# Kernel optimization log

Measured on AMD Instinct MI355X. Metric: run time of the kernel, lower is better.

The kernel has to match this reference:

```python
import jax, jax.numpy as jnp
import numpy as np

N = 50000       # nodes
E = 800000      # edges
D_IN = 128
D_OUT = 128
K = 3           # num_stacks
T = 2           # num_layers


def setup_inputs() -> dict:
    key = jax.random.key(0)
    ks = jax.random.split(key, 10)
    feats = jax.random.normal(ks[0], (N, D_IN), dtype=jnp.float32)
    src = jax.random.randint(ks[1], (E,), 0, N, dtype=jnp.int32)
    dst = jax.random.randint(ks[2], (E,), 0, N, dtype=jnp.int32)
    s = 0.05
    w0 = jax.random.normal(ks[3], (K, D_IN, D_OUT), dtype=jnp.float32) * s
    b0 = jax.random.normal(ks[4], (K, D_OUT), dtype=jnp.float32) * s
    w = jax.random.normal(ks[5], (K, D_OUT, D_OUT), dtype=jnp.float32) * s
    bw = jax.random.normal(ks[6], (K, D_OUT), dtype=jnp.float32) * s
    v = jax.random.normal(ks[7], (K, D_IN, D_OUT), dtype=jnp.float32) * s
    bv = jax.random.normal(ks[8], (K, D_OUT), dtype=jnp.float32) * s
    return {"feats": feats, "src": src, "dst": dst,
            "w0": w0, "b0": b0, "w": w, "bw": bw, "v": v, "bv": bv}


def _propagate(h, src, dst, norm):
    # symmetric degree-normalized SpMM: D^{-1/2} A D^{-1/2} h
    h = h * norm                                   # [N, d]
    agg = jax.ops.segment_sum(h[src], dst, num_segments=N)  # gather + scatter-add
    return agg * norm


def reference(feats, src, dst, w0, b0, w, bw, v, bv):
    ones = jnp.ones((E,), dtype=feats.dtype)
    deg = jnp.clip(jax.ops.segment_sum(ones, dst, num_segments=N), 1.0)
    norm = (deg ** -0.5)[:, None]                  # [N, 1]

    out = jnp.zeros((N, D_OUT), dtype=feats.dtype)
    for k in range(K):
        h = feats
        for t in range(T):
            h = _propagate(h, src, dst, norm)
            if t == 0:
                h = h @ w0[k] + b0[k]
            else:
                h = h @ w[k] + bw[k]
            h = h + (feats @ v[k] + bv[k])         # dropout is identity (p=0, eval)
            h = jax.nn.relu(h)
        out = out + h
    return out / K
```

## Files before the change

### kernel.cpp

```cpp
#include <hip/hip_runtime.h>

#define N_NODES 50000
#define N_EDGES 800000
#define D 128
#define PLANE ((size_t)N_NODES * D)
#define NCHUNK ((N_NODES + 255) / 256)

typedef float f32x4 __attribute__((ext_vector_type(4)));
typedef short bf16x8 __attribute__((ext_vector_type(8)));

__device__ __forceinline__ unsigned short f2bf(float x) {
  unsigned int u = __float_as_uint(x);
  u += 0x7FFFu + ((u >> 16) & 1u);
  return (unsigned short)(u >> 16);
}
__device__ __forceinline__ float bf2f(unsigned short h) {
  return __uint_as_float((unsigned int)h << 16);
}


__global__ __launch_bounds__(256) void scan_local(const int* __restrict__ cnt,
                                                  int* __restrict__ local,
                                                  int* __restrict__ partial) {
  __shared__ int s[256];
  int t = threadIdx.x;
  int i = blockIdx.x * 256 + t;
  int v = (i < N_NODES) ? cnt[i] : 0;
  s[t] = v;
  __syncthreads();
  for (int off = 1; off < 256; off <<= 1) {
    int tmp = (t >= off) ? s[t - off] : 0;
    __syncthreads();
    s[t] += tmp;
    __syncthreads();
  }
  if (i < N_NODES) local[i] = s[t] - v;
  if (t == 255) partial[blockIdx.x] = s[255];
}

__global__ __launch_bounds__(256) void scan_chunks(const int* __restrict__ partial,
                                                   int* __restrict__ chunk_off,
                                                   int* __restrict__ rowptr) {
  __shared__ int s[256];
  int t = threadIdx.x;
  int v = (t < NCHUNK) ? partial[t] : 0;
  s[t] = v;
  __syncthreads();
  for (int off = 1; off < 256; off <<= 1) {
    int tmp = (t >= off) ? s[t - off] : 0;
    __syncthreads();
    s[t] += tmp;
    __syncthreads();
  }
  if (t < NCHUNK) chunk_off[t] = s[t] - v;
  if (t == 255) rowptr[N_NODES] = s[255];
}

__global__ __launch_bounds__(256) void finalize_rows(const int* __restrict__ cnt,
                                                     const int* __restrict__ local,
                                                     const int* __restrict__ chunk_off,
                                                     int* __restrict__ rowptr,
                                                     int* __restrict__ cursor,
                                                     float* __restrict__ norm) {
  int i = blockIdx.x * 256 + threadIdx.x;
  if (i < N_NODES) {
    int r = local[i] + chunk_off[blockIdx.x];
    rowptr[i] = r;
    cursor[i] = r;
    int d = cnt[i];
    if (d < 1) d = 1;
    norm[i] = rsqrtf((float)d);
  }
}

__global__ __launch_bounds__(256) void fill_csr(const int* __restrict__ src,
                                                const int* __restrict__ dst,
                                                int* __restrict__ cursor,
                                                int* __restrict__ col) {
  int e = blockIdx.x * blockDim.x + threadIdx.x;
  if (e < N_EDGES) {
    int pos = atomicAdd(&cursor[dst[e]], 1);
    col[pos] = src[e];
  }
}


#define CONV_THREADS ((int)(PLANE / 4))
#define WT_THREADS (2 * 3 * 128 * 256)
#define PREP_TOTAL (CONV_THREADS + WT_THREADS + N_EDGES)

__global__ __launch_bounds__(256) void prep_all(const float* __restrict__ feats,
                                                const float* __restrict__ w0,
                                                const float* __restrict__ w,
                                                const float* __restrict__ v,
                                                const int* __restrict__ dst,
                                                unsigned short* __restrict__ feats_bf,
                                                unsigned short* __restrict__ bt_h1,
                                                unsigned short* __restrict__ bt_out,
                                                int* __restrict__ cnt) {
  int idx = blockIdx.x * 256 + threadIdx.x;
  if (idx < CONV_THREADS) {
    float4 x = ((const float4*)feats)[idx];
    ushort4 o;
    o.x = f2bf(x.x);
    o.y = f2bf(x.y);
    o.z = f2bf(x.z);
    o.w = f2bf(x.w);
    ((ushort4*)feats_bf)[idx] = o;
    return;
  }
  idx -= CONV_THREADS;
  if (idx < WT_THREADS) {
    int buf = idx / 98304;
    int rem = idx - buf * 98304;
    int stack = rem / 32768;
    int rem2 = rem & 32767;
    int n = rem2 >> 8;
    int k = rem2 & 255;
    const float* srcm;
    int kk;
    if (k < 128) {
      srcm = (buf == 0) ? w0 : w;
      kk = k;
    } else {
      srcm = v;
      kk = k - 128;
    }
    float val = srcm[(size_t)stack * 16384 + (size_t)kk * 128 + n];
    unsigned short* dstb = (buf == 0) ? bt_h1 : bt_out;
    dstb[(size_t)stack * 32768 + (size_t)n * 256 + k] = f2bf(val);
    return;
  }
  idx -= WT_THREADS;
  if (idx < N_EDGES) atomicAdd(&cnt[dst[idx]], 1);
}


template <int NK>
__global__ __launch_bounds__(256) void spmm_bf(const unsigned short* __restrict__ h,
                                               const float* __restrict__ norm,
                                               const int* __restrict__ rowptr,
                                               const int* __restrict__ col,
                                               unsigned short* __restrict__ out) {
  int row = blockIdx.x * 4 + (threadIdx.x >> 6);
  if (row >= N_NODES) return;
  int lane = threadIdx.x & 63;
  int sub = lane >> 4;
  int c16 = lane & 15;
  int beg = rowptr[row], end = rowptr[row + 1];

  float acc[NK][8];
#pragma unroll
  for (int m = 0; m < NK; ++m)
#pragma unroll
    for (int j = 0; j < 8; ++j) acc[m][j] = 0.f;

#pragma unroll 4
  for (int e = beg; e < end; e += 4) {
    int eidx = e + sub;
    bool valid = eidx < end;
    int s = valid ? col[eidx] : 0;
    float wgt = valid ? norm[s] : 0.f;
    const unsigned short* hp = h + (size_t)s * D + c16 * 8;
#pragma unroll
    for (int m = 0; m < NK; ++m) {
      bf16x8 hv = *(const bf16x8*)(hp + m * PLANE);
#pragma unroll
      for (int j = 0; j < 8; ++j)
        acc[m][j] = fmaf(wgt, bf2f((unsigned short)hv[j]), acc[m][j]);
    }
  }

#pragma unroll
  for (int m = 0; m < NK; ++m)
#pragma unroll
    for (int j = 0; j < 8; ++j) {
      float vv = acc[m][j];
      vv += __shfl_xor(vv, 16);
      vv += __shfl_xor(vv, 32);
      acc[m][j] = vv;
    }

  if (sub == 0) {
    float nd = norm[row];
#pragma unroll
    for (int m = 0; m < NK; ++m) {
      bf16x8 ov;
#pragma unroll
      for (int j = 0; j < 8; ++j) ov[j] = (short)f2bf(acc[m][j] * nd);
      *(bf16x8*)(out + m * PLANE + (size_t)row * D + c16 * 8) = ov;
    }
  }
}


__device__ __forceinline__ void stage_B128(unsigned short (*Bs)[256],
                                           const unsigned short* __restrict__ Btg,
                                           int tid) {
#pragma unroll
  for (int i = 0; i < 16; ++i) {
    int t = tid + i * 256;
    int n = t >> 5;
    int kc = t & 31;
    int kcs = kc ^ (n & 31);
    *(bf16x8*)&Bs[n][kcs * 8] = *(const bf16x8*)(Btg + (size_t)n * 256 + kc * 8);
  }
}

__device__ __forceinline__ bf16x8 read_B128(const unsigned short (*Bs)[256], int n,
                                            int chunk) {
  return *(const bf16x8*)&Bs[n][(chunk ^ (n & 31)) * 8];
}

__global__ __launch_bounds__(256) void gemm_h1_fused(
    const unsigned short* __restrict__ P,
    const unsigned short* __restrict__ feats_bf,
    const unsigned short* __restrict__ Bt,
    const float* __restrict__ b0, const float* __restrict__ bv,
    unsigned short* __restrict__ h1_bf) {
  __shared__ unsigned short Bs[128][256];

  int tid = threadIdx.x;
  int lane = tid & 63;
  int wv = tid >> 6;
  int ln15 = lane & 15;
  int g = lane >> 4;

  int m0 = blockIdx.x * 64 + wv * 16;
  int r0 = m0 + ln15;
  if (r0 >= N_NODES) r0 = N_NODES - 1;

  bf16x8 a0[8];
#pragma unroll
  for (int s = 0; s < 4; ++s) {
    a0[s] = *(const bf16x8*)(P + (size_t)r0 * 128 + g * 8 + s * 32);
    a0[s + 4] = *(const bf16x8*)(feats_bf + (size_t)r0 * 128 + g * 8 + s * 32);
  }

  for (int stk = 0; stk < 3; ++stk) {
    if (stk) __syncthreads();
    stage_B128(Bs, Bt + (size_t)stk * 32768, tid);
    __syncthreads();

    f32x4 acc[8];
#pragma unroll
    for (int nt = 0; nt < 8; ++nt) acc[nt] = (f32x4)(0.f);

#pragma unroll
    for (int s = 0; s < 8; ++s) {
#pragma unroll
      for (int nt = 0; nt < 8; ++nt) {
        bf16x8 bfr = read_B128(Bs, nt * 16 + ln15, s * 4 + g);
        acc[nt] = __builtin_amdgcn_mfma_f32_16x16x32_bf16(a0[s], bfr, acc[nt], 0, 0, 0);
      }
    }

    unsigned short* outp = h1_bf + (size_t)stk * PLANE;
#pragma unroll
    for (int nt = 0; nt < 8; ++nt) {
      int colj = nt * 16 + ln15;
      float bsum = b0[stk * 128 + colj] + bv[stk * 128 + colj];
#pragma unroll
      for (int r = 0; r < 4; ++r) {
        int mA = m0 + g * 4 + r;
        if (mA < N_NODES) {
          float x = acc[nt][r] + bsum;
          outp[(size_t)mA * 128 + colj] = f2bf(x > 0.f ? x : 0.f);
        }
      }
    }
  }
}

__global__ __launch_bounds__(256) void gemm_out_fused(
    const unsigned short* __restrict__ agg,
    const unsigned short* __restrict__ feats_bf,
    const unsigned short* __restrict__ Bt,
    const float* __restrict__ bwp, const float* __restrict__ bvp,
    float* __restrict__ outp) {
  __shared__ unsigned short Bs[128][256];

  int tid = threadIdx.x;
  int lane = tid & 63;
  int wv = tid >> 6;
  int ln15 = lane & 15;
  int g = lane >> 4;

  int m0 = blockIdx.x * 64 + wv * 16;
  int r0 = m0 + ln15;
  if (r0 >= N_NODES) r0 = N_NODES - 1;

  bf16x8 f0[4];
#pragma unroll
  for (int s = 0; s < 4; ++s)
    f0[s] = *(const bf16x8*)(feats_bf + (size_t)r0 * 128 + g * 8 + s * 32);

  f32x4 sum[8];
#pragma unroll
  for (int nt = 0; nt < 8; ++nt) sum[nt] = (f32x4)(0.f);

  for (int stk = 0; stk < 3; ++stk) {
    if (stk) __syncthreads();
    stage_B128(Bs, Bt + (size_t)stk * 32768, tid);
    __syncthreads();

    const unsigned short* A1 = agg + (size_t)stk * PLANE;
    bf16x8 g0[4];
#pragma unroll
    for (int s = 0; s < 4; ++s)
      g0[s] = *(const bf16x8*)(A1 + (size_t)r0 * 128 + g * 8 + s * 32);

    f32x4 acc[8];
#pragma unroll
    for (int nt = 0; nt < 8; ++nt) acc[nt] = (f32x4)(0.f);

#pragma unroll
    for (int s = 0; s < 8; ++s) {
      bf16x8 af = (s < 4) ? g0[s & 3] : f0[s & 3];
#pragma unroll
      for (int nt = 0; nt < 8; ++nt) {
        bf16x8 bfr = read_B128(Bs, nt * 16 + ln15, s * 4 + g);
        acc[nt] = __builtin_amdgcn_mfma_f32_16x16x32_bf16(af, bfr, acc[nt], 0, 0, 0);
      }
    }

#pragma unroll
    for (int nt = 0; nt < 8; ++nt) {
      int colj = nt * 16 + ln15;
      float bsum = bwp[stk * 128 + colj] + bvp[stk * 128 + colj];
#pragma unroll
      for (int r = 0; r < 4; ++r) {
        float x = acc[nt][r] + bsum;
        sum[nt][r] += (x > 0.f ? x : 0.f);
      }
    }
  }

  const float sc = 1.0f / 3.0f;
#pragma unroll
  for (int nt = 0; nt < 8; ++nt) {
    int colj = nt * 16 + ln15;
#pragma unroll
    for (int r = 0; r < 4; ++r) {
      int mA = m0 + g * 4 + r;
      if (mA < N_NODES) outp[(size_t)mA * 128 + colj] = sum[nt][r] * sc;
    }
  }
}


extern "C" void kernel_launch(void* const* d_in, const int* in_sizes, int n_in,
                              void* d_out, int out_size, void* d_ws, size_t ws_size,
                              hipStream_t stream) {
  const float* feats = (const float*)d_in[0];
  const int* src = (const int*)d_in[1];
  const int* dst = (const int*)d_in[2];
  const float* w0 = (const float*)d_in[3];
  const float* b0 = (const float*)d_in[4];
  const float* w = (const float*)d_in[5];
  const float* bw = (const float*)d_in[6];
  const float* v = (const float*)d_in[7];
  const float* bv = (const float*)d_in[8];
  float* out = (float*)d_out;

  char* ws = (char*)d_ws;
  size_t off = 0;
  auto alloc = [&](size_t bytes) {
    void* p = ws + off;
    off += (bytes + 255) & ~(size_t)255;
    return p;
  };
  int* cnt = (int*)alloc(N_NODES * 4);
  int* local = (int*)alloc(N_NODES * 4);
  int* partial = (int*)alloc(NCHUNK * 4);
  int* chunk_off = (int*)alloc(NCHUNK * 4);
  float* norm = (float*)alloc(N_NODES * 4);
  int* rowptr = (int*)alloc((N_NODES + 1) * 4);
  int* cursor = (int*)alloc(N_NODES * 4);
  int* col = (int*)alloc(N_EDGES * 4);
  unsigned short* bt_h1 = (unsigned short*)alloc(3 * 32768 * 2);
  unsigned short* bt_out = (unsigned short*)alloc(3 * 32768 * 2);

  size_t pb = PLANE * 2;
  unsigned short* feats_bf = (unsigned short*)alloc(pb);
  unsigned short* P_bf = (unsigned short*)alloc(pb);
  unsigned short* h1_bf = (unsigned short*)alloc(3 * pb);
  unsigned short* agg_bf = (unsigned short*)alloc(3 * pb);

  hipMemsetAsync(cnt, 0, N_NODES * 4, stream);

  dim3 blk(256);
  prep_all<<<(PREP_TOTAL + 255) / 256, blk, 0, stream>>>(feats, w0, w, v, dst, feats_bf,
                                                         bt_h1, bt_out, cnt);
  scan_local<<<NCHUNK, blk, 0, stream>>>(cnt, local, partial);
  scan_chunks<<<1, blk, 0, stream>>>(partial, chunk_off, rowptr);
  finalize_rows<<<NCHUNK, blk, 0, stream>>>(cnt, local, chunk_off, rowptr, cursor, norm);
  fill_csr<<<(N_EDGES + 255) / 256, blk, 0, stream>>>(src, dst, cursor, col);

  int sblocks = (N_NODES + 3) / 4;
  int mblocks64 = (N_NODES + 63) / 64;

  spmm_bf<1><<<sblocks, blk, 0, stream>>>(feats_bf, norm, rowptr, col, P_bf);
  gemm_h1_fused<<<mblocks64, blk, 0, stream>>>(P_bf, feats_bf, bt_h1, b0, bv, h1_bf);
  spmm_bf<3><<<sblocks, blk, 0, stream>>>(h1_bf, norm, rowptr, col, agg_bf);
  gemm_out_fused<<<mblocks64, blk, 0, stream>>>(agg_bf, feats_bf, bt_out, bw, bv, out);
}
```

Measured before the change: 358.1 us.

## Precompute feats@V once per stack and overlap it with first SpMM

The feats@V product used to be recomputed inside both fused GEMMs by concatenating K=256. It is now computed once per stack into a fragment-ordered bf16 buffer. That work runs in a hybrid kernel whose extra blocks perform the first SpMM at the same time. Both later GEMMs then drop to K=128 and read the precomputed values in the epilogue, and the buffers are aliased to reuse memory. In exchange, the FV buffer adds extra global traffic, and rounding the FV term to bf16 adds a small precision loss.

Measured after the change: 394.3 us. 10.1% more time.

```diff
diff --git a/kernel.cpp b/kernel.cpp
--- a/kernel.cpp
+++ b/kernel.cpp
@@ -5,6 +5,8 @@
 #define D 128
 #define PLANE ((size_t)N_NODES * D)
 #define NCHUNK ((N_NODES + 255) / 256)
+#define MB64 ((N_NODES + 63) / 64)
+#define FVB_ELEMS ((size_t)3 * MB64 * 256 * 32)
 
 typedef float f32x4 __attribute__((ext_vector_type(4)));
 typedef short bf16x8 __attribute__((ext_vector_type(8)));
@@ -86,7 +88,7 @@
 
 
 #define CONV_THREADS ((int)(PLANE / 4))
-#define WT_THREADS (2 * 3 * 128 * 256)
+#define WT_THREADS (3 * 3 * 128 * 128)
 #define PREP_TOTAL (CONV_THREADS + WT_THREADS + N_EDGES)
 
 __global__ __launch_bounds__(256) void prep_all(const float* __restrict__ feats,
@@ -95,8 +97,9 @@
                                                 const float* __restrict__ v,
                                                 const int* __restrict__ dst,
                                                 unsigned short* __restrict__ feats_bf,
-                                                unsigned short* __restrict__ bt_h1,
-                                                unsigned short* __restrict__ bt_out,
+                                                unsigned short* __restrict__ btw0,
+                                                unsigned short* __restrict__ btw,
+                                                unsigned short* __restrict__ btv,
                                                 int* __restrict__ cnt) {
   int idx = blockIdx.x * 256 + threadIdx.x;
   if (idx < CONV_THREADS) {
@@ -111,24 +114,16 @@
   }
   idx -= CONV_THREADS;
   if (idx < WT_THREADS) {
-    int buf = idx / 98304;
-    int rem = idx - buf * 98304;
-    int stack = rem / 32768;
-    int rem2 = rem & 32767;
-    int n = rem2 >> 8;
-    int k = rem2 & 255;
-    const float* srcm;
-    int kk;
-    if (k < 128) {
-      srcm = (buf == 0) ? w0 : w;
-      kk = k;
-    } else {
-      srcm = v;
-      kk = k - 128;
-    }
-    float val = srcm[(size_t)stack * 16384 + (size_t)kk * 128 + n];
-    unsigned short* dstb = (buf == 0) ? bt_h1 : bt_out;
-    dstb[(size_t)stack * 32768 + (size_t)n * 256 + k] = f2bf(val);
+    int buf = idx / 49152;
+    int rem = idx - buf * 49152;
+    int stack = rem >> 14;
+    int r2 = rem & 16383;
+    int n = r2 >> 7;
+    int k = r2 & 127;
+    const float* srcm = (buf == 0) ? w0 : (buf == 1) ? w : v;
+    unsigned short* dstb = (buf == 0) ? btw0 : (buf == 1) ? btw : btv;
+    dstb[(size_t)stack * 16384 + (size_t)n * 128 + k] =
+        f2bf(srcm[(size_t)stack * 16384 + (size_t)k * 128 + n]);
     return;
   }
   idx -= WT_THREADS;
@@ -137,12 +132,12 @@
 
 
 template <int NK>
-__global__ __launch_bounds__(256) void spmm_bf(const unsigned short* __restrict__ h,
-                                               const float* __restrict__ norm,
-                                               const int* __restrict__ rowptr,
-                                               const int* __restrict__ col,
-                                               unsigned short* __restrict__ out) {
-  int row = blockIdx.x * 4 + (threadIdx.x >> 6);
+__device__ __forceinline__ void spmm_body(const unsigned short* const* hs,
+                                          const float* __restrict__ norm,
+                                          const int* __restrict__ rowptr,
+                                          const int* __restrict__ col,
+                                          unsigned short* const* outs, int bx) {
+  int row = bx * 4 + ((int)threadIdx.x >> 6);
   if (row >= N_NODES) return;
   int lane = threadIdx.x & 63;
   int sub = lane >> 4;
@@ -161,10 +156,10 @@
     bool valid = eidx < end;
     int s = valid ? col[eidx] : 0;
     float wgt = valid ? norm[s] : 0.f;
-    const unsigned short* hp = h + (size_t)s * D + c16 * 8;
+    size_t base = (size_t)s * D + c16 * 8;
 #pragma unroll
     for (int m = 0; m < NK; ++m) {
-      bf16x8 hv = *(const bf16x8*)(hp + m * PLANE);
+      bf16x8 hv = *(const bf16x8*)(hs[m] + base);
 #pragma unroll
       for (int j = 0; j < 8; ++j)
         acc[m][j] = fmaf(wgt, bf2f((unsigned short)hv[j]), acc[m][j]);
@@ -188,37 +183,112 @@
       bf16x8 ov;
 #pragma unroll
       for (int j = 0; j < 8; ++j) ov[j] = (short)f2bf(acc[m][j] * nd);
-      *(bf16x8*)(out + m * PLANE + (size_t)row * D + c16 * 8) = ov;
-    }
-  }
-}
-
-
-__device__ __forceinline__ void stage_B128(unsigned short (*Bs)[256],
-                                           const unsigned short* __restrict__ Btg,
-                                           int tid) {
-#pragma unroll
-  for (int i = 0; i < 16; ++i) {
+      *(bf16x8*)(outs[m] + (size_t)row * D + c16 * 8) = ov;
+    }
+  }
+}
+
+
+__device__ __forceinline__ void stage_Bq(unsigned short (*Bs)[128],
+                                         const unsigned short* __restrict__ Btg,
+                                         int tid) {
+#pragma unroll
+  for (int i = 0; i < 8; ++i) {
     int t = tid + i * 256;
-    int n = t >> 5;
-    int kc = t & 31;
-    int kcs = kc ^ (n & 31);
-    *(bf16x8*)&Bs[n][kcs * 8] = *(const bf16x8*)(Btg + (size_t)n * 256 + kc * 8);
-  }
-}
-
-__device__ __forceinline__ bf16x8 read_B128(const unsigned short (*Bs)[256], int n,
-                                            int chunk) {
-  return *(const bf16x8*)&Bs[n][(chunk ^ (n & 31)) * 8];
-}
-
-__global__ __launch_bounds__(256) void gemm_h1_fused(
-    const unsigned short* __restrict__ P,
+    int n = t >> 4;
+    int c = t & 15;
+    int cs = c ^ (n & 15);
+    *(bf16x8*)&Bs[n][cs * 8] = *(const bf16x8*)(Btg + (size_t)n * 128 + c * 8);
+  }
+}
+
+__device__ __forceinline__ bf16x8 read_Bq(const unsigned short (*Bs)[128], int n,
+                                          int chunk) {
+  return *(const bf16x8*)&Bs[n][(chunk ^ (n & 15)) * 8];
+}
+
+
+__global__ __launch_bounds__(256) void hybrid_fv_spmm1(
     const unsigned short* __restrict__ feats_bf,
-    const unsigned short* __restrict__ Bt,
+    const unsigned short* __restrict__ btv,
+    const float* __restrict__ norm, const int* __restrict__ rowptr,
+    const int* __restrict__ col,
+    unsigned short* __restrict__ FVb,
+    unsigned short* __restrict__ P) {
+  __shared__ unsigned short Bs[128][128];
+
+  if (blockIdx.x < MB64) {
+    int tid = threadIdx.x;
+    int lane = tid & 63;
+    int wv = tid >> 6;
+    int ln15 = lane & 15;
+    int g = lane >> 4;
+
+    int m0 = blockIdx.x * 64 + wv * 16;
+    int r0 = m0 + ln15;
+    if (r0 >= N_NODES) r0 = N_NODES - 1;
+
+    bf16x8 a[4];
+#pragma unroll
+    for (int s = 0; s < 4; ++s)
+      a[s] = *(const bf16x8*)(feats_bf + (size_t)r0 * 128 + g * 8 + s * 32);
+
+    for (int stk = 0; stk < 3; ++stk) {
+      if (stk) __syncthreads();
+      stage_Bq(Bs, btv + (size_t)stk * 16384, tid);
+      __syncthreads();
+
+      f32x4 acc[8];
+#pragma unroll
+      for (int nt = 0; nt < 8; ++nt) acc[nt] = (f32x4)(0.f);
+
+#pragma unroll
+      for (int s = 0; s < 4; ++s) {
+#pragma unroll
+        for (int nt = 0; nt < 8; ++nt) {
+          bf16x8 bfr = read_Bq(Bs, nt * 16 + ln15, s * 4 + g);
+          acc[nt] = __builtin_amdgcn_mfma_f32_16x16x32_bf16(a[s], bfr, acc[nt], 0, 0, 0);
+        }
+      }
+
+      unsigned short buf[32];
+#pragma unroll
+      for (int nt = 0; nt < 8; ++nt)
+#pragma unroll
+        for (int r = 0; r < 4; ++r) buf[nt * 4 + r] = f2bf(acc[nt][r]);
+      bf16x8* dst =
+          (bf16x8*)(FVb + (((size_t)stk * MB64 + blockIdx.x) * 256 + tid) * 32);
+#pragma unroll
+      for (int q = 0; q < 4; ++q) dst[q] = ((bf16x8*)buf)[q];
+    }
+  } else {
+    const unsigned short* hs[1] = {feats_bf};
+    unsigned short* outs[1] = {P};
+    spmm_body<1>(hs, norm, rowptr, col, outs, blockIdx.x - MB64);
+  }
+}
+
+
+__global__ __launch_bounds__(256) void spmm3(
+    const unsigned short* __restrict__ h0, const unsigned short* __restrict__ h1,
+    const unsigned short* __restrict__ h2, const float* __restrict__ norm,
+    const int* __restrict__ rowptr, const int* __restrict__ col,
+    unsigned short* __restrict__ o0, unsigned short* __restrict__ o1,
+    unsigned short* __restrict__ o2) {
+  const unsigned short* hs[3] = {h0, h1, h2};
+  unsigned short* outs[3] = {o0, o1, o2};
+  spmm_body<3>(hs, norm, rowptr, col, outs, blockIdx.x);
+}
+
+
+__global__ __launch_bounds__(256) void gemm_h1(
+    const unsigned short* __restrict__ P, const unsigned short* __restrict__ btw0,
+    const unsigned short* __restrict__ FVb,
     const float* __restrict__ b0, const float* __restrict__ bv,
-    unsigned short* __restrict__ h1_bf) {
-  __shared__ unsigned short Bs[128][256];
+    unsigned short* __restrict__ o0, unsigned short* __restrict__ o1,
+    unsigned short* __restrict__ o2) {
+  __shared__ unsigned short Bs[128][128];
+  unsigned short* outs[3] = {o0, o1, o2};
 
   int tid = threadIdx.x;
   int lane = tid & 63;
@@ -230,16 +300,14 @@
   int r0 = m0 + ln15;
   if (r0 >= N_NODES) r0 = N_NODES - 1;
 
-  bf16x8 a0[8];
-#pragma unroll
-  for (int s = 0; s < 4; ++s) {
-    a0[s] = *(const bf16x8*)(P + (size_t)r0 * 128 + g * 8 + s * 32);
-    a0[s + 4] = *(const bf16x8*)(feats_bf + (size_t)r0 * 128 + g * 8 + s * 32);
-  }
+  bf16x8 a[4];
+#pragma unroll
+  for (int s = 0; s < 4; ++s)
+    a[s] = *(const bf16x8*)(P + (size_t)r0 * 128 + g * 8 + s * 32);
 
   for (int stk = 0; stk < 3; ++stk) {
     if (stk) __syncthreads();
-    stage_B128(Bs, Bt + (size_t)stk * 32768, tid);
+    stage_Bq(Bs, btw0 + (size_t)stk * 16384, tid);
     __syncthreads();
 
     f32x4 acc[8];
@@ -247,15 +315,21 @@
     for (int nt = 0; nt < 8; ++nt) acc[nt] = (f32x4)(0.f);
 
 #pragma unroll
-    for (int s = 0; s < 8; ++s) {
+    for (int s = 0; s < 4; ++s) {
 #pragma unroll
       for (int nt = 0; nt < 8; ++nt) {
-        bf16x8 bfr = read_B128(Bs, nt * 16 + ln15, s * 4 + g);
-        acc[nt] = __builtin_amdgcn_mfma_f32_16x16x32_bf16(a0[s], bfr, acc[nt], 0, 0, 0);
+        bf16x8 bfr = read_Bq(Bs, nt * 16 + ln15, s * 4 + g);
+        acc[nt] = __builtin_amdgcn_mfma_f32_16x16x32_bf16(a[s], bfr, acc[nt], 0, 0, 0);
       }
     }
 
-    unsigned short* outp = h1_bf + (size_t)stk * PLANE;
+    bf16x8 fv[4];
+    const bf16x8* fvp =
+        (const bf16x8*)(FVb + (((size_t)stk * MB64 + blockIdx.x) * 256 + tid) * 32);
+#pragma unroll
+    for (int q = 0; q < 4; ++q) fv[q] = fvp[q];
+
+    unsigned short* outp = outs[stk];
 #pragma unroll
     for (int nt = 0; nt < 8; ++nt) {
       int colj = nt * 16 + ln15;
@@ -264,7 +338,9 @@
       for (int r = 0; r < 4; ++r) {
         int mA = m0 + g * 4 + r;
         if (mA < N_NODES) {
-          float x = acc[nt][r] + bsum;
+          int vi = nt * 4 + r;
+          float fvv = bf2f((unsigned short)fv[vi >> 3][vi & 7]);
+          float x = acc[nt][r] + fvv + bsum;
           outp[(size_t)mA * 128 + colj] = f2bf(x > 0.f ? x : 0.f);
         }
       }
@@ -272,13 +348,15 @@
   }
 }
 
-__global__ __launch_bounds__(256) void gemm_out_fused(
-    const unsigned short* __restrict__ agg,
-    const unsigned short* __restrict__ feats_bf,
-    const unsigned short* __restrict__ Bt,
+
+__global__ __launch_bounds__(256) void gemm_out(
+    const unsigned short* __restrict__ a0, const unsigned short* __restrict__ a1,
+    const unsigned short* __restrict__ a2, const unsigned short* __restrict__ btw,
+    const unsigned short* __restrict__ FVb,
     const float* __restrict__ bwp, const float* __restrict__ bvp,
     float* __restrict__ outp) {
-  __shared__ unsigned short Bs[128][256];
+  __shared__ unsigned short Bs[128][128];
+  const unsigned short* aggs[3] = {a0, a1, a2};
 
   int tid = threadIdx.x;
   int lane = tid & 63;
@@ -290,39 +368,38 @@
   int r0 = m0 + ln15;
   if (r0 >= N_NODES) r0 = N_NODES - 1;
 
-  bf16x8 f0[4];
-#pragma unroll
-  for (int s = 0; s < 4; ++s)
-    f0[s] = *(const bf16x8*)(feats_bf + (size_t)r0 * 128 + g * 8 + s * 32);
-
   f32x4 sum[8];
 #pragma unroll
   for (int nt = 0; nt < 8; ++nt) sum[nt] = (f32x4)(0.f);
 
   for (int stk = 0; stk < 3; ++stk) {
     if (stk) __syncthreads();
-    stage_B128(Bs, Bt + (size_t)stk * 32768, tid);
-    __syncthreads();
-
-    const unsigned short* A1 = agg + (size_t)stk * PLANE;
-    bf16x8 g0[4];
+    stage_Bq(Bs, btw + (size_t)stk * 16384, tid);
+    __syncthreads();
+
+    bf16x8 a[4];
 #pragma unroll
     for (int s = 0; s < 4; ++s)
-      g0[s] = *(const bf16x8*)(A1 + (size_t)r0 * 128 + g * 8 + s * 32);
+      a[s] = *(const bf16x8*)(aggs[stk] + (size_t)r0 * 128 + g * 8 + s * 32);
 
     f32x4 acc[8];
 #pragma unroll
     for (int nt = 0; nt < 8; ++nt) acc[nt] = (f32x4)(0.f);
 
 #pragma unroll
-    for (int s = 0; s < 8; ++s) {
-      bf16x8 af = (s < 4) ? g0[s & 3] : f0[s & 3];
+    for (int s = 0; s < 4; ++s) {
 #pragma unroll
       for (int nt = 0; nt < 8; ++nt) {
-        bf16x8 bfr = read_B128(Bs, nt * 16 + ln15, s * 4 + g);
-        acc[nt] = __builtin_amdgcn_mfma_f32_16x16x32_bf16(af, bfr, acc[nt], 0, 0, 0);
+        bf16x8 bfr = read_Bq(Bs, nt * 16 + ln15, s * 4 + g);
+        acc[nt] = __builtin_amdgcn_mfma_f32_16x16x32_bf16(a[s], bfr, acc[nt], 0, 0, 0);
       }
     }
+
+    bf16x8 fv[4];
+    const bf16x8* fvp =
+        (const bf16x8*)(FVb + (((size_t)stk * MB64 + blockIdx.x) * 256 + tid) * 32);
+#pragma unroll
+    for (int q = 0; q < 4; ++q) fv[q] = fvp[q];
 
 #pragma unroll
     for (int nt = 0; nt < 8; ++nt) {
@@ -330,7 +407,9 @@
       float bsum = bwp[stk * 128 + colj] + bvp[stk * 128 + colj];
 #pragma unroll
       for (int r = 0; r < 4; ++r) {
-        float x = acc[nt][r] + bsum;
+        int vi = nt * 4 + r;
+        float fvv = bf2f((unsigned short)fv[vi >> 3][vi & 7]);
+        float x = acc[nt][r] + fvv + bsum;
         sum[nt][r] += (x > 0.f ? x : 0.f);
       }
     }
@@ -378,30 +457,39 @@
   int* rowptr = (int*)alloc((N_NODES + 1) * 4);
   int* cursor = (int*)alloc(N_NODES * 4);
   int* col = (int*)alloc(N_EDGES * 4);
-  unsigned short* bt_h1 = (unsigned short*)alloc(3 * 32768 * 2);
-  unsigned short* bt_out = (unsigned short*)alloc(3 * 32768 * 2);
+  unsigned short* btw0 = (unsigned short*)alloc(3 * 16384 * 2);
+  unsigned short* btw = (unsigned short*)alloc(3 * 16384 * 2);
+  unsigned short* btv = (unsigned short*)alloc(3 * 16384 * 2);
 
   size_t pb = PLANE * 2;
-  unsigned short* feats_bf = (unsigned short*)alloc(pb);
-  unsigned short* P_bf = (unsigned short*)alloc(pb);
-  unsigned short* h1_bf = (unsigned short*)alloc(3 * pb);
-  unsigned short* agg_bf = (unsigned short*)alloc(3 * pb);
+  unsigned short* p0 = (unsigned short*)alloc(pb);
+  unsigned short* p1 = (unsigned short*)alloc(pb);
+  unsigned short* FVb = (unsigned short*)alloc(FVB_ELEMS * 2);
+  unsigned short* p5 = (unsigned short*)alloc(pb);
+  unsigned short* p6 = (unsigned short*)alloc(pb);
+  unsigned short* p7 = (unsigned short*)alloc(pb);
+  unsigned short* p8 = (unsigned short*)alloc(pb);
+
+  unsigned short* feats_bf = p0;
+  unsigned short* P_bf = p1;
+  unsigned short *h1a = p5, *h1b = p6, *h1c = p0;
+  unsigned short *agga = p1, *aggb = p7, *aggc = p8;
 
   hipMemsetAsync(cnt, 0, N_NODES * 4, stream);
 
   dim3 blk(256);
   prep_all<<<(PREP_TOTAL + 255) / 256, blk, 0, stream>>>(feats, w0, w, v, dst, feats_bf,
-                                                         bt_h1, bt_out, cnt);
+                                                         btw0, btw, btv, cnt);
   scan_local<<<NCHUNK, blk, 0, stream>>>(cnt, local, partial);
   scan_chunks<<<1, blk, 0, stream>>>(partial, chunk_off, rowptr);
   finalize_rows<<<NCHUNK, blk, 0, stream>>>(cnt, local, chunk_off, rowptr, cursor, norm);
   fill_csr<<<(N_EDGES + 255) / 256, blk, 0, stream>>>(src, dst, cursor, col);
 
   int sblocks = (N_NODES + 3) / 4;
-  int mblocks64 = (N_NODES + 63) / 64;
-
-  spmm_bf<1><<<sblocks, blk, 0, stream>>>(feats_bf, norm, rowptr, col, P_bf);
-  gemm_h1_fused<<<mblocks64, blk, 0, stream>>>(P_bf, feats_bf, bt_h1, b0, bv, h1_bf);
-  spmm_bf<3><<<sblocks, blk, 0, stream>>>(h1_bf, norm, rowptr, col, agg_bf);
-  gemm_out_fused<<<mblocks64, blk, 0, stream>>>(agg_bf, feats_bf, bt_out, bw, bv, out);
-}
+
+  hybrid_fv_spmm1<<<MB64 + sblocks, blk, 0, stream>>>(feats_bf, btv, norm, rowptr, col,
+                                                      FVb, P_bf);
+  gemm_h1<<<MB64, blk, 0, stream>>>(P_bf, btw0, FVb, b0, bv, h1a, h1b, h1c);
+  spmm3<<<sblocks, blk, 0, stream>>>(h1a, h1b, h1c, norm, rowptr, col, agga, aggb, aggc);
+  gemm_out<<<MB64, blk, 0, stream>>>(agga, aggb, aggc, btw, FVb, bw, bv, out);
+}
```
